# Optimization experiments

Hardware: AMD Instinct MI355X
Metric: run time of the kernel (lower is better)

Reference implementation:

```python
import jax, jax.numpy as jnp
import numpy as np

EMB_DIM = 1024
NUM_HEADS = 16
HEAD_DIM = EMB_DIM // NUM_HEADS  # 64
B, S = 2, 2048


def setup_inputs() -> dict:
    key = jax.random.key(0)
    ks = jax.random.split(key, 9)
    scale = 1.0 / np.sqrt(EMB_DIM)
    return {
        "query": jax.random.normal(ks[0], (B, S, EMB_DIM), dtype=jnp.float32),
        "Wq": jax.random.normal(ks[1], (EMB_DIM, EMB_DIM), dtype=jnp.float32) * scale,
        "bq": jax.random.normal(ks[2], (EMB_DIM,), dtype=jnp.float32) * 0.01,
        "Wk": jax.random.normal(ks[3], (EMB_DIM, EMB_DIM), dtype=jnp.float32) * scale,
        "bk": jax.random.normal(ks[4], (EMB_DIM,), dtype=jnp.float32) * 0.01,
        "Wv": jax.random.normal(ks[5], (EMB_DIM, EMB_DIM), dtype=jnp.float32) * scale,
        "bv": jax.random.normal(ks[6], (EMB_DIM,), dtype=jnp.float32) * 0.01,
        "Wo": jax.random.normal(ks[7], (EMB_DIM, EMB_DIM), dtype=jnp.float32) * scale,
        "bo": jax.random.normal(ks[8], (EMB_DIM,), dtype=jnp.float32) * 0.01,
    }


def reference(query, Wq, bq, Wk, bk, Wv, bv, Wo, bo):
    # Self-attention path (key_value=None, mask=None in the original forward).
    b, s, _ = query.shape
    # torch nn.Linear: y = x @ W.T + b
    def proj(x, W, bias):
        y = jnp.einsum('bse,fe->bsf', x, W) + bias
        # [B,S,E] -> [B,H,S,D]
        return y.reshape(b, s, NUM_HEADS, HEAD_DIM).transpose(0, 2, 1, 3)

    q = proj(query, Wq, bq)
    k = proj(query, Wk, bk)
    v = proj(query, Wv, bv)

    scores = jnp.einsum('bhqd,bhkd->bhqk', q, k) / np.sqrt(HEAD_DIM).astype(np.float32)
    attn = jax.nn.softmax(scores, axis=-1)  # [B,H,S,S]
    out = jnp.einsum('bhqk,bhkd->bhqd', attn, v)
    out = out.transpose(0, 2, 1, 3).reshape(b, s, EMB_DIM)
    return jnp.einsum('bse,fe->bsf', out, Wo) + bo
```

## Files before the change

### kernel.cpp

```cpp
#include <hip/hip_runtime.h>
#include <hip/hip_bf16.h>

using bf16x4 = __attribute__((ext_vector_type(4))) short;
using short8 = __attribute__((ext_vector_type(8))) short;
using f32x4  = __attribute__((ext_vector_type(4))) float;
using u32x2  = __attribute__((ext_vector_type(2))) unsigned;

__device__ __forceinline__ short f2bf(float f) {
  unsigned u = __builtin_bit_cast(unsigned, f);
  u = (u + 0x7fffu + ((u >> 16) & 1u)) >> 16;
  return (short)u;
}
__device__ __forceinline__ unsigned pk2(float a, float b) {
  __hip_bfloat162 h = __float22bfloat162_rn(make_float2(a, b));
  unsigned u; __builtin_memcpy(&u, &h, 4);
  return u;
}
__device__ __forceinline__ void gload16(const short* g, short* l) {
  __builtin_amdgcn_global_load_lds(
      (const __attribute__((address_space(1))) unsigned int*)g,
      (__attribute__((address_space(3))) unsigned int*)l, 16, 0, 0);
}

constexpr int E  = 1024;
constexpr int SL = 2048;
constexpr int NB = 2;
constexpr int NH = 16;
constexpr int M  = NB * SL;

__global__ __launch_bounds__(256) void convert_kernel(
    const float* __restrict__ X,  const float* __restrict__ Wq,
    const float* __restrict__ Wk, const float* __restrict__ Wv,
    const float* __restrict__ Wo, short* __restrict__ out)
{
  const size_t i8 = ((size_t)blockIdx.x * 256 + threadIdx.x) * 8;
  const float* src;
  if (i8 < (size_t)(4u << 20)) {
    src = X + i8;
  } else {
    size_t r = i8 - (size_t)(4u << 20);
    int wi = (int)(r >> 20);
    size_t off = r & ((1u << 20) - 1);
    src = (wi == 0 ? Wq : wi == 1 ? Wk : wi == 2 ? Wv : Wo) + off;
  }
  f32x4 a = *(const f32x4*)src;
  f32x4 b = *(const f32x4*)(src + 4);
  short hb[8];
#pragma unroll
  for (int e = 0; e < 4; ++e) { hb[e] = f2bf(a[e]); hb[4 + e] = f2bf(b[e]); }
  *(short8*)(out + i8) = *(short8*)hb;
}

template <int TM, int TN, bool OUTF32, bool FUSEV>
__global__ __launch_bounds__(256) void gemm_kernel(
    const short* __restrict__ A0, const short* __restrict__ A1, const short* __restrict__ A2,
    const short* __restrict__ W0, const short* __restrict__ W1, const short* __restrict__ W2,
    const float* __restrict__ b0, const float* __restrict__ b1, const float* __restrict__ b2,
    void* __restrict__ Y0, void* __restrict__ Y1, void* __restrict__ Y2,
    float s0, float s1, float s2, int ld0, int ld1, int ld2)
{
  constexpr int BK = 32;
  constexpr int RA = TM / 64;
  constexpr int RB = TN / 64;
  constexpr int WM = TM / 2, WN = TN / 2;
  constexpr int NI = WM / 16, NJ = WN / 16;
  __shared__ alignas(16) short As[2][TM * BK];
  __shared__ alignas(16) short Bs[2][TN * BK];
  const int t = threadIdx.x;
  const int l = t & 63;
  const int w = t >> 6;
  const int c = l & 15;
  const int g = l >> 4;
  const int z = blockIdx.z;
  const short* Ap = (z == 0) ? A0 : (z == 1) ? A1 : A2;
  const short* Wp = (z == 0) ? W0 : (z == 1) ? W1 : W2;
  const float* bp = (z == 0) ? b0 : (z == 1) ? b1 : b2;
  void* Yp        = (z == 0) ? Y0 : (z == 1) ? Y1 : Y2;
  const float sc  = (z == 0) ? s0 : (z == 1) ? s1 : s2;
  const int ldY   = (z == 0) ? ld0 : (z == 1) ? ld1 : ld2;
  const bool vtr  = FUSEV && (z == 2);
  const int m0 = (vtr ? blockIdx.y : blockIdx.x) * TM;
  const int n0 = (vtr ? blockIdx.x : blockIdx.y) * TN;

  const short* gA[RA]; int oA[RA];
  const short* gB[RB]; int oB[RB];
#pragma unroll
  for (int r = 0; r < RA; ++r) {
    const int cc = r * 256 + t;
    gA[r] = Ap + (size_t)(m0 + (cc >> 2)) * E + (cc & 3) * 8;
    oA[r] = (r * 256 + (t & ~63)) * 8;
  }
#pragma unroll
  for (int r = 0; r < RB; ++r) {
    const int cc = r * 256 + t;
    gB[r] = Wp + (size_t)(n0 + (cc >> 2)) * E + (cc & 3) * 8;
    oB[r] = (r * 256 + (t & ~63)) * 8;
  }

#pragma unroll
  for (int r = 0; r < RA; ++r) gload16(gA[r], &As[0][oA[r]]);
#pragma unroll
  for (int r = 0; r < RB; ++r) gload16(gB[r], &Bs[0][oB[r]]);

  const int wm = (w >> 1) * WM;
  const int wn = (w & 1) * WN;
  f32x4 acc[NI][NJ] = {};
  int cur = 0;

  for (int k0 = 0; k0 < E; k0 += BK) {
    __syncthreads();
    if (k0 + BK < E) {
#pragma unroll
      for (int r = 0; r < RA; ++r) gload16(gA[r] + k0 + BK, &As[cur ^ 1][oA[r]]);
#pragma unroll
      for (int r = 0; r < RB; ++r) gload16(gB[r] + k0 + BK, &Bs[cur ^ 1][oB[r]]);
    }
    short8 ah[NI], bfr[NJ];
#pragma unroll
    for (int i = 0; i < NI; ++i)
      ah[i] = *(const short8*)&As[cur][(wm + i * 16 + c) * BK + g * 8];
#pragma unroll
    for (int j = 0; j < NJ; ++j)
      bfr[j] = *(const short8*)&Bs[cur][(wn + j * 16 + c) * BK + g * 8];
#pragma unroll
    for (int i = 0; i < NI; ++i)
#pragma unroll
      for (int j = 0; j < NJ; ++j)
        acc[i][j] = __builtin_amdgcn_mfma_f32_16x16x32_bf16(ah[i], bfr[j], acc[i][j], 0, 0, 0);
    cur ^= 1;
  }

#pragma unroll
  for (int j = 0; j < NJ; ++j) {
    const int col = n0 + wn + j * 16 + c;
    const float bcol = vtr ? 0.f : bp[col];
#pragma unroll
    for (int i = 0; i < NI; ++i) {
      const int rowb = m0 + wm + i * 16 + g * 4;
#pragma unroll
      for (int r = 0; r < 4; ++r) {
        const int row = rowb + r;
        const float bias = vtr ? bp[row] : bcol;
        const float v = (acc[i][j][r] + bias) * sc;
        if (OUTF32) ((float*)Yp)[(size_t)row * ldY + col] = v;
        else        ((short*)Yp)[(size_t)row * ldY + col] = f2bf(v);
      }
    }
  }
}

__global__ __launch_bounds__(512) void flash_kernel(
    const short* __restrict__ Qm, const short* __restrict__ Km,
    const short* __restrict__ VTm, short* __restrict__ Oh)
{
  __shared__ alignas(16) short Ks[64][72];
  __shared__ alignas(16) short Vt[64][72];
  __shared__ alignas(16) short Pl[8][16][72];
  const int t = threadIdx.x;
  const int l = t & 63;
  const int w = t >> 6;
  const int c = l & 15;
  const int g = l >> 4;
  const int q0 = blockIdx.x * 128;
  const int bh = (int)blockIdx.y;
  const int b = bh >> 4;
  const int h = bh & 15;
  const size_t baseK = (size_t)b * SL * E + h * 64;
  const size_t baseV = (size_t)(h * 64) * M + (size_t)b * SL;

  short8 aq[2];
  {
    const short* qp = Qm + baseK + (size_t)(q0 + w * 16 + c) * E + g * 8;
    aq[0] = *(const short8*)qp;
    aq[1] = *(const short8*)(qp + 32);
  }

  f32x4 lacc = {0.f, 0.f, 0.f, 0.f};
  f32x4 acc_o[4] = {};

  const int srow = t >> 3, sseg = t & 7;
  const short* gK = Km + baseK + (size_t)srow * E + sseg * 8;
  const short* gV = VTm + baseV + (size_t)srow * M + sseg * 8;

  short8 kreg = *(const short8*)gK;
  short8 vreg = *(const short8*)gV;

  constexpr int NT = SL / 64;
  for (int kt = 0; kt < NT; ++kt) {
    __syncthreads();
    *(short8*)&Ks[srow][sseg * 8] = kreg;
    *(short8*)&Vt[srow][sseg * 8] = vreg;
    __syncthreads();
    if (kt + 1 < NT) {
      kreg = *(const short8*)(gK + (size_t)(kt + 1) * 64 * E);
      vreg = *(const short8*)(gV + (kt + 1) * 64);
    }

    f32x4 st[4] = {};
#pragma unroll
    for (int j = 0; j < 4; ++j)
#pragma unroll
      for (int kc = 0; kc < 2; ++kc) {
        short8 kf = *(const short8*)&Ks[j * 16 + c][kc * 32 + g * 8];
        st[j] = __builtin_amdgcn_mfma_f32_16x16x32_bf16(kf, aq[kc], st[j], 0, 0, 0);
      }

#pragma unroll
    for (int j = 0; j < 4; ++j) {
      f32x4 p;
#pragma unroll
      for (int r = 0; r < 4; ++r) p[r] = __builtin_amdgcn_exp2f(st[j][r]);
      lacc += p;
      u32x2 pk = {pk2(p[0], p[1]), pk2(p[2], p[3])};
      *(u32x2*)&Pl[w][c][j * 16 + g * 4] = pk;
    }
    short8 ap[2];
    ap[0] = *(const short8*)&Pl[w][c][g * 8];
    ap[1] = *(const short8*)&Pl[w][c][32 + g * 8];

#pragma unroll
    for (int j = 0; j < 4; ++j)
#pragma unroll
      for (int kc = 0; kc < 2; ++kc) {
        short8 vf = *(const short8*)&Vt[j * 16 + c][kc * 32 + g * 8];
        acc_o[j] = __builtin_amdgcn_mfma_f32_16x16x32_bf16(vf, ap[kc], acc_o[j], 0, 0, 0);
      }
  }

  float s = lacc[0] + lacc[1] + lacc[2] + lacc[3];
  s += __shfl_xor(s, 16);
  s += __shfl_xor(s, 32);
  const float inv = 1.0f / s;

  const int token = q0 + w * 16 + c;
  const size_t obase = ((size_t)b * SL + token) * E + h * 64;
#pragma unroll
  for (int j = 0; j < 4; ++j) {
    u32x2 o2 = {pk2(acc_o[j][0] * inv, acc_o[j][1] * inv),
                pk2(acc_o[j][2] * inv, acc_o[j][3] * inv)};
    *(u32x2*)(Oh + obase + j * 16 + g * 4) = o2;
  }
}

extern "C" void kernel_launch(void* const* d_in, const int* in_sizes, int n_in,
                              void* d_out, int out_size, void* d_ws, size_t ws_size,
                              hipStream_t stream)
{
  const float* X  = (const float*)d_in[0];
  const float* Wq = (const float*)d_in[1];
  const float* bq = (const float*)d_in[2];
  const float* Wk = (const float*)d_in[3];
  const float* bk = (const float*)d_in[4];
  const float* Wv = (const float*)d_in[5];
  const float* bv = (const float*)d_in[6];
  const float* Wo = (const float*)d_in[7];
  const float* bo = (const float*)d_in[8];
  float* out = (float*)d_out;

  const size_t szX = (size_t)M * E;
  const size_t szW = (size_t)E * E;
  short* Xb  = (short*)d_ws;
  short* Wqb = Xb + szX;
  short* Wkb = Wqb + szW;
  short* Wvb = Wkb + szW;
  short* Wob = Wvb + szW;
  short* Qw  = Wob + szW;
  short* Kw  = Qw + szX;
  short* VTw = Kw + szX;

  convert_kernel<<<4096, 256, 0, stream>>>(X, Wq, Wk, Wv, Wo, Xb);

  const float kLog2eOver8 = 0.18033688011112042f;
  dim3 g1(M / 128, E / 128, 3);
  gemm_kernel<128, 128, false, true><<<g1, 256, 0, stream>>>(
      Xb, Xb, Wvb,
      Wqb, Wkb, Xb,
      bq, bk, bv,
      (void*)Qw, (void*)Kw, (void*)VTw,
      kLog2eOver8, 1.0f, 1.0f, E, E, M);

  dim3 g2(SL / 128, NB * NH);
  flash_kernel<<<g2, 512, 0, stream>>>(Qw, Kw, VTw, Qw );

  dim3 g3(M / 128, E / 64, 1);
  gemm_kernel<128, 64, true, false><<<g3, 256, 0, stream>>>(
      Qw, Qw, Qw,
      Wob, Wob, Wob,
      bo, bo, bo,
      (void*)out, (void*)out, (void*)out,
      1.0f, 1.0f, 1.0f, E, E, E);
}
```

Measured before the change: 211.2 us.

## Rewrite flash attention with 32x32 MFMA, register P transpose, double-buffered swizzled LDS

The flash kernel moves from 16x16x32 to 32x32x16 bf16 MFMA, with each wave now owning 32 query rows and 4 waves per block instead of 8. The P matrix is re-laid out in registers with v_permlane32_swap instead of a round trip through LDS. K and V tiles are double-buffered in XOR-swizzled LDS, which avoids bank conflicts and halves the barriers per tile. The aim is to raise MFMA efficiency and cut LDS traffic and synchronisation, at the cost of higher register pressure from the 16-wide accumulators.

```diff
diff --git a/kernel.cpp b/kernel.cpp
--- a/kernel.cpp
+++ b/kernel.cpp
@@ -4,6 +4,7 @@
 using bf16x4 = __attribute__((ext_vector_type(4))) short;
 using short8 = __attribute__((ext_vector_type(8))) short;
 using f32x4  = __attribute__((ext_vector_type(4))) float;
+using f32x16 = __attribute__((ext_vector_type(16))) float;
 using u32x2  = __attribute__((ext_vector_type(2))) unsigned;
 
 __device__ __forceinline__ short f2bf(float f) {
@@ -20,6 +21,9 @@
   __builtin_amdgcn_global_load_lds(
       (const __attribute__((address_space(1))) unsigned int*)g,
       (__attribute__((address_space(3))) unsigned int*)l, 16, 0, 0);
+}
+__device__ __forceinline__ void pl32swap(unsigned &a, unsigned &b) {
+  asm("v_permlane32_swap_b32 %0, %1" : "+v"(a), "+v"(b));
 }
 
 constexpr int E  = 1024;
@@ -149,96 +153,135 @@
   }
 }
 
-__global__ __launch_bounds__(512) void flash_kernel(
+__global__ __launch_bounds__(256, 2) void flash_kernel(
     const short* __restrict__ Qm, const short* __restrict__ Km,
     const short* __restrict__ VTm, short* __restrict__ Oh)
 {
-  __shared__ alignas(16) short Ks[64][72];
-  __shared__ alignas(16) short Vt[64][72];
-  __shared__ alignas(16) short Pl[8][16][72];
+  __shared__ alignas(16) short Ks[2][64][64];
+  __shared__ alignas(16) short Vt[2][64][64];
   const int t = threadIdx.x;
   const int l = t & 63;
   const int w = t >> 6;
-  const int c = l & 15;
-  const int g = l >> 4;
+  const int c = l & 31;
+  const int hi = l >> 5;
   const int q0 = blockIdx.x * 128;
   const int bh = (int)blockIdx.y;
-  const int b = bh >> 4;
+  const int bat = bh >> 4;
   const int h = bh & 15;
-  const size_t baseK = (size_t)b * SL * E + h * 64;
-  const size_t baseV = (size_t)(h * 64) * M + (size_t)b * SL;
-
-  short8 aq[2];
+  const size_t baseK = (size_t)bat * SL * E + h * 64;
+  const size_t baseV = (size_t)(h * 64) * M + (size_t)bat * SL;
+
+  short8 qf[4];
   {
-    const short* qp = Qm + baseK + (size_t)(q0 + w * 16 + c) * E + g * 8;
-    aq[0] = *(const short8*)qp;
-    aq[1] = *(const short8*)(qp + 32);
-  }
-
+    const short* qp = Qm + baseK + (size_t)(q0 + w * 32 + c) * E + hi * 8;
+#pragma unroll
+    for (int tt = 0; tt < 4; ++tt) qf[tt] = *(const short8*)(qp + tt * 16);
+  }
+
+  const int sr = t >> 3, sg = t & 7;
+  const int swz = (sg ^ (sr & 7)) * 8;
+  const short* gK0 = Km + baseK + (size_t)sr * E + sg * 8;
+  const short* gK1 = gK0 + (size_t)32 * E;
+  const short* gV0 = VTm + baseV + (size_t)sr * M + sg * 8;
+  const short* gV1 = gV0 + (size_t)32 * M;
+  const int wo0 = sr * 64 + swz;
+  const int wo1 = (sr + 32) * 64 + swz;
+
+  short8 k0r, k1r, v0r, v1r;
+  k0r = *(const short8*)gK0; k1r = *(const short8*)gK1;
+  v0r = *(const short8*)gV0; v1r = *(const short8*)gV1;
+  *(short8*)(&Ks[0][0][0] + wo0) = k0r; *(short8*)(&Ks[0][0][0] + wo1) = k1r;
+  *(short8*)(&Vt[0][0][0] + wo0) = v0r; *(short8*)(&Vt[0][0][0] + wo1) = v1r;
+  k0r = *(const short8*)(gK0 + (size_t)64 * E);
+  k1r = *(const short8*)(gK1 + (size_t)64 * E);
+  v0r = *(const short8*)(gV0 + 64);
+  v1r = *(const short8*)(gV1 + 64);
+
+  f32x16 oa0 = {}, oa1 = {};
   f32x4 lacc = {0.f, 0.f, 0.f, 0.f};
-  f32x4 acc_o[4] = {};
-
-  const int srow = t >> 3, sseg = t & 7;
-  const short* gK = Km + baseK + (size_t)srow * E + sseg * 8;
-  const short* gV = VTm + baseV + (size_t)srow * M + sseg * 8;
-
-  short8 kreg = *(const short8*)gK;
-  short8 vreg = *(const short8*)gV;
-
-  constexpr int NT = SL / 64;
-  for (int kt = 0; kt < NT; ++kt) {
+  __syncthreads();
+
+  constexpr int NTT = SL / 64;
+  const int sx = c & 7;
+  for (int kt = 0; kt < NTT; ++kt) {
+    const int cur = kt & 1;
+    if (kt + 1 < NTT) {
+      short* Kn = &Ks[cur ^ 1][0][0];
+      short* Vn = &Vt[cur ^ 1][0][0];
+      *(short8*)(Kn + wo0) = k0r; *(short8*)(Kn + wo1) = k1r;
+      *(short8*)(Vn + wo0) = v0r; *(short8*)(Vn + wo1) = v1r;
+      if (kt + 2 < NTT) {
+        const size_t ko = (size_t)(kt + 2) * 64 * E;
+        const int vo = (kt + 2) * 64;
+        k0r = *(const short8*)(gK0 + ko); k1r = *(const short8*)(gK1 + ko);
+        v0r = *(const short8*)(gV0 + vo); v1r = *(const short8*)(gV1 + vo);
+      }
+    }
+    const short* Kc0 = &Ks[cur][c][0];
+    const short* Kc1 = &Ks[cur][32 + c][0];
+    const short* Vc0 = &Vt[cur][c][0];
+    const short* Vc1 = &Vt[cur][32 + c][0];
+
+    f32x16 st0 = {}, st1 = {};
+#pragma unroll
+    for (int tt = 0; tt < 4; ++tt) {
+      const int off = ((tt * 2 + hi) ^ sx) * 8;
+      short8 kf0 = *(const short8*)(Kc0 + off);
+      short8 kf1 = *(const short8*)(Kc1 + off);
+      st0 = __builtin_amdgcn_mfma_f32_32x32x16_bf16(kf0, qf[tt], st0, 0, 0, 0);
+      st1 = __builtin_amdgcn_mfma_f32_32x32x16_bf16(kf1, qf[tt], st1, 0, 0, 0);
+    }
+
+    float p0[16], p1[16];
+#pragma unroll
+    for (int i = 0; i < 16; ++i) p0[i] = __builtin_amdgcn_exp2f(st0[i]);
+#pragma unroll
+    for (int i = 0; i < 16; ++i) p1[i] = __builtin_amdgcn_exp2f(st1[i]);
+#pragma unroll
+    for (int i = 0; i < 16; ++i) lacc[i & 3] += p0[i] + p1[i];
+
+    unsigned W0[4][2], W1[4][2];
+#pragma unroll
+    for (int b8 = 0; b8 < 4; ++b8) {
+      W0[b8][0] = pk2(p0[4 * b8 + 0], p0[4 * b8 + 1]);
+      W0[b8][1] = pk2(p0[4 * b8 + 2], p0[4 * b8 + 3]);
+      W1[b8][0] = pk2(p1[4 * b8 + 0], p1[4 * b8 + 1]);
+      W1[b8][1] = pk2(p1[4 * b8 + 2], p1[4 * b8 + 3]);
+    }
+
+#pragma unroll
+    for (int tt = 0; tt < 4; ++tt) {
+      unsigned a0, a1, b0, b1;
+      if (tt == 0)      { a0 = W0[0][0]; a1 = W0[0][1]; b0 = W0[1][0]; b1 = W0[1][1]; }
+      else if (tt == 1) { a0 = W0[2][0]; a1 = W0[2][1]; b0 = W0[3][0]; b1 = W0[3][1]; }
+      else if (tt == 2) { a0 = W1[0][0]; a1 = W1[0][1]; b0 = W1[1][0]; b1 = W1[1][1]; }
+      else              { a0 = W1[2][0]; a1 = W1[2][1]; b0 = W1[3][0]; b1 = W1[3][1]; }
+      pl32swap(a0, b0);
+      pl32swap(a1, b1);
+      union { unsigned u[4]; short8 s8; } pf;
+      pf.u[0] = a0; pf.u[1] = a1; pf.u[2] = b0; pf.u[3] = b1;
+      const int off = ((tt * 2 + hi) ^ sx) * 8;
+      short8 vf0 = *(const short8*)(Vc0 + off);
+      short8 vf1 = *(const short8*)(Vc1 + off);
+      oa0 = __builtin_amdgcn_mfma_f32_32x32x16_bf16(vf0, pf.s8, oa0, 0, 0, 0);
+      oa1 = __builtin_amdgcn_mfma_f32_32x32x16_bf16(vf1, pf.s8, oa1, 0, 0, 0);
+    }
     __syncthreads();
-    *(short8*)&Ks[srow][sseg * 8] = kreg;
-    *(short8*)&Vt[srow][sseg * 8] = vreg;
-    __syncthreads();
-    if (kt + 1 < NT) {
-      kreg = *(const short8*)(gK + (size_t)(kt + 1) * 64 * E);
-      vreg = *(const short8*)(gV + (kt + 1) * 64);
-    }
-
-    f32x4 st[4] = {};
-#pragma unroll
-    for (int j = 0; j < 4; ++j)
-#pragma unroll
-      for (int kc = 0; kc < 2; ++kc) {
-        short8 kf = *(const short8*)&Ks[j * 16 + c][kc * 32 + g * 8];
-        st[j] = __builtin_amdgcn_mfma_f32_16x16x32_bf16(kf, aq[kc], st[j], 0, 0, 0);
-      }
-
-#pragma unroll
-    for (int j = 0; j < 4; ++j) {
-      f32x4 p;
-#pragma unroll
-      for (int r = 0; r < 4; ++r) p[r] = __builtin_amdgcn_exp2f(st[j][r]);
-      lacc += p;
-      u32x2 pk = {pk2(p[0], p[1]), pk2(p[2], p[3])};
-      *(u32x2*)&Pl[w][c][j * 16 + g * 4] = pk;
-    }
-    short8 ap[2];
-    ap[0] = *(const short8*)&Pl[w][c][g * 8];
-    ap[1] = *(const short8*)&Pl[w][c][32 + g * 8];
-
-#pragma unroll
-    for (int j = 0; j < 4; ++j)
-#pragma unroll
-      for (int kc = 0; kc < 2; ++kc) {
-        short8 vf = *(const short8*)&Vt[j * 16 + c][kc * 32 + g * 8];
-        acc_o[j] = __builtin_amdgcn_mfma_f32_16x16x32_bf16(vf, ap[kc], acc_o[j], 0, 0, 0);
-      }
   }
 
   float s = lacc[0] + lacc[1] + lacc[2] + lacc[3];
-  s += __shfl_xor(s, 16);
   s += __shfl_xor(s, 32);
   const float inv = 1.0f / s;
-
-  const int token = q0 + w * 16 + c;
-  const size_t obase = ((size_t)b * SL + token) * E + h * 64;
-#pragma unroll
-  for (int j = 0; j < 4; ++j) {
-    u32x2 o2 = {pk2(acc_o[j][0] * inv, acc_o[j][1] * inv),
-                pk2(acc_o[j][2] * inv, acc_o[j][3] * inv)};
-    *(u32x2*)(Oh + obase + j * 16 + g * 4) = o2;
+  const int q = q0 + w * 32 + c;
+  short* op = Oh + ((size_t)bat * SL + q) * E + h * 64 + hi * 4;
+#pragma unroll
+  for (int b8 = 0; b8 < 4; ++b8) {
+    u32x2 t0 = {pk2(oa0[4 * b8 + 0] * inv, oa0[4 * b8 + 1] * inv),
+                pk2(oa0[4 * b8 + 2] * inv, oa0[4 * b8 + 3] * inv)};
+    *(u32x2*)(op + b8 * 8) = t0;
+    u32x2 t1 = {pk2(oa1[4 * b8 + 0] * inv, oa1[4 * b8 + 1] * inv),
+                pk2(oa1[4 * b8 + 2] * inv, oa1[4 * b8 + 3] * inv)};
+    *(u32x2*)(op + 32 + b8 * 8) = t1;
   }
 }
 
@@ -280,7 +323,7 @@
       kLog2eOver8, 1.0f, 1.0f, E, E, M);
 
   dim3 g2(SL / 128, NB * NH);
-  flash_kernel<<<g2, 512, 0, stream>>>(Qw, Kw, VTw, Qw );
+  flash_kernel<<<g2, 256, 0, stream>>>(Qw, Kw, VTw, Qw );
 
   dim3 g3(M / 128, E / 64, 1);
   gemm_kernel<128, 64, true, false><<<g3, 256, 0, stream>>>(
```

New measurement: 206.6 us. 1.02x faster.
